# Performance work log

Hardware: AMD Instinct MI355X
Metric: run time of the kernel (lower is better)

Reference implementation:

```python
import jax, jax.numpy as jnp
import numpy as np

DIM = 1024
HID = 2048
E = 8      # num_experts
K = 2      # num_experts_per_tok


def setup_inputs() -> dict:
    key = jax.random.key(0)
    ks = jax.random.split(key, 5)
    s_in = 1.0 / np.sqrt(DIM)
    s_hid = 1.0 / np.sqrt(HID)
    x = jax.random.normal(ks[0], (2, 2048, DIM), dtype=jnp.float32)
    Wg = jax.random.uniform(ks[1], (DIM, E), minval=-s_in, maxval=s_in, dtype=jnp.float32)
    W1 = jax.random.uniform(ks[2], (E, DIM, HID), minval=-s_in, maxval=s_in, dtype=jnp.float32)
    W3 = jax.random.uniform(ks[3], (E, DIM, HID), minval=-s_in, maxval=s_in, dtype=jnp.float32)
    W2 = jax.random.uniform(ks[4], (E, HID, DIM), minval=-s_hid, maxval=s_hid, dtype=jnp.float32)
    return {"x": x, "Wg": Wg, "W1": W1, "W3": W3, "W2": W2}


def reference(x, Wg, W1, W3, W2):
    orig_shape = x.shape
    xt = x.reshape(-1, x.shape[-1])            # [T, D]
    T = xt.shape[0]
    scores = xt @ Wg                            # [T, E] (gate_softmax=False)
    ew, ei = jax.lax.top_k(scores, K)           # [T, K]
    ew = jax.nn.softmax(ew, axis=-1)            # softmax over selected experts
    # combine weights: [T, E], zero for unselected experts
    combine = jnp.zeros((T, E), dtype=xt.dtype)
    combine = combine.at[jnp.arange(T)[:, None], ei].add(ew)
    out = jnp.zeros_like(xt)
    for e in range(E):  # fixed small loop over structurally distinct experts
        h = jax.nn.silu(xt @ W1[e]) * (xt @ W3[e])   # [T, HID] SwiGLU
        out = out + combine[:, e:e + 1] * (h @ W2[e])
    return out.reshape(orig_shape)
```

## Files before the change

### kernel.cpp

```cpp
#include <hip/hip_runtime.h>

typedef unsigned short u16;
typedef unsigned int u32;
using bf16x8 = __attribute__((ext_vector_type(8))) __bf16;
using f32x4  = __attribute__((ext_vector_type(4))) float;

#define T_TOK 4096
#define DIMD  1024
#define HIDN  2048
#define NEXP  8
#define NSLOT (2 * T_TOK)

#define OFF_CNT  0
#define OFF_TCNT 64
#define OFF_TOK  16448
#define OFF_WGT  (OFF_TOK + NEXP*T_TOK*4)
#define OFF_T2S  (OFF_WGT + NEXP*T_TOK*4)
#define OFF_XB   (1<<20)
#define SZ_XB    (T_TOK*DIMD*2)
#define OFF_W1T  (OFF_XB + SZ_XB)
#define SZ_W     (NEXP*DIMD*HIDN*2)
#define OFF_W3T  (OFF_W1T + SZ_W)
#define OFF_W2T  (OFF_W3T + SZ_W)
#define OFF_H    (OFF_W2T + SZ_W)
#define OFF_OS   OFF_W1T

__device__ __forceinline__ u16 f2bf(float f) {
    u32 u = __float_as_uint(f);
    u32 r = (u + 0x7fff + ((u >> 16) & 1)) >> 16;
    return (u16)r;
}

__device__ __forceinline__ void gl2lds16(const void* g, void* l) {
    __builtin_amdgcn_global_load_lds(
        (__attribute__((address_space(1))) void*)(g),
        (__attribute__((address_space(3))) void*)(l),
        16, 0, 0);
}

__device__ __forceinline__ bf16x8 ldfrag(const u16* base, int r, int s, int q) {
    int idx = r * 64 + ((((s << 2) | q) ^ (r & 7)) << 3);
    union { uint4 u; bf16x8 b; } c;
    c.u = *(const uint4*)(base + idx);
    return c.b;
}

__device__ __forceinline__ int prefix_cnt(const int* cnt, int e) {
    int b = 0;
#pragma unroll
    for (int j = 0; j < NEXP; j++) b += (j < e) ? cnt[j] : 0;
    return b;
}

__global__ __launch_bounds__(256) void gate_kernel(
    const float* __restrict__ x, const float* __restrict__ wg,
    int* __restrict__ cnt, int* __restrict__ tok, float* __restrict__ wgt,
    u16* __restrict__ xb)
{
    int t = blockIdx.x * 4 + (threadIdx.x >> 6);
    int lane = threadIdx.x & 63;
    float s[8];
#pragma unroll
    for (int e = 0; e < 8; e++) s[e] = 0.f;
    const float* xr = x + (size_t)t * DIMD;
    u16* xbr = xb + (size_t)t * DIMD;
#pragma unroll
    for (int i = 0; i < 16; i++) {
        int d = i * 64 + lane;
        float xv = xr[d];
        xbr[d] = f2bf(xv);
        float4 w0 = *(const float4*)(wg + d * 8);
        float4 w1 = *(const float4*)(wg + d * 8 + 4);
        s[0] += xv * w0.x; s[1] += xv * w0.y;
        s[2] += xv * w0.z; s[3] += xv * w0.w;
        s[4] += xv * w1.x; s[5] += xv * w1.y;
        s[6] += xv * w1.z; s[7] += xv * w1.w;
    }
#pragma unroll
    for (int e = 0; e < 8; e++)
        for (int off = 32; off; off >>= 1) s[e] += __shfl_xor(s[e], off, 64);
    if (lane == 0) {
        int e0 = 0; float b0 = s[0];
        for (int e = 1; e < 8; e++) if (s[e] > b0) { b0 = s[e]; e0 = e; }
        int e1 = (e0 == 0) ? 1 : 0; float b1 = s[e1];
        for (int e = 0; e < 8; e++) if (e != e0 && s[e] > b1) { b1 = s[e]; e1 = e; }
        float ex = __expf(b1 - b0);
        float w0 = 1.f / (1.f + ex);
        float w1 = ex / (1.f + ex);
        int p0 = atomicAdd(&cnt[e0], 1);
        tok[e0 * T_TOK + p0] = t; wgt[e0 * T_TOK + p0] = w0;
        int p1 = atomicAdd(&cnt[e1], 1);
        tok[e1 * T_TOK + p1] = t; wgt[e1 * T_TOK + p1] = w1;
    }
}

__global__ __launch_bounds__(256) void map_kernel(
    const int* __restrict__ cnt, const int* __restrict__ tok,
    int* __restrict__ tcnt, int* __restrict__ t2s)
{
    int gid = blockIdx.x * 256 + threadIdx.x;
    int e = gid >> 12, i = gid & 4095;
    if (i >= cnt[e]) return;
    int base = prefix_cnt(cnt, e);
    int t = tok[e * T_TOK + i];
    int idx = atomicAdd(&tcnt[t], 1);
    t2s[2 * t + idx] = base + i;
}

__global__ __launch_bounds__(256) void wtr_kernel(
    const float* __restrict__ w1, u16* __restrict__ w1t,
    const float* __restrict__ w3, u16* __restrict__ w3t,
    const float* __restrict__ w2, u16* __restrict__ w2t)
{
    __shared__ float Lf[64 * 64];
    int bid = blockIdx.x;
    int tz = bid >> 9;
    int tt = bid & 511;
    int e = tz & 7;
    const float* in; u16* out; int K, N, kt, ntl;
    if (tz < 16) {
        in = (tz < 8) ? w1 : w3; out = (tz < 8) ? w1t : w3t;
        K = DIMD; N = HIDN; kt = tt >> 5; ntl = tt & 31;
    } else {
        in = w2; out = w2t;
        K = HIDN; N = DIMD; kt = tt >> 4; ntl = tt & 15;
    }
    int k0 = kt * 64, n0 = ntl * 64;
    const float* ip = in + (size_t)e * K * N;
    u16* op = out + (size_t)e * K * N;

    int tid = threadIdx.x;
    int wbase = tid & ~63;
#pragma unroll
    for (int i = 0; i < 4; i++) {
        int slot = i * 256 + tid;
        int r = slot >> 4, cb = slot & 15;
        gl2lds16(ip + (size_t)(k0 + r) * N + n0 + cb * 4,
                 Lf + (i * 256 + wbase) * 4);
    }
    __syncthreads();

    int w = tid >> 6, lane = tid & 63;
    union { u16 s[16]; uint4 q[2]; } u;
#pragma unroll
    for (int i = 0; i < 16; i++)
        u.s[i] = f2bf(Lf[(w * 16 + i) * 64 + lane]);
    uint4* dst = (uint4*)(op + (size_t)(n0 + lane) * K + k0 + w * 16);
    dst[0] = u.q[0]; dst[1] = u.q[1];
}

__global__ __launch_bounds__(256, 3) void gemm1_kernel(
    const u16* __restrict__ xb, const u16* __restrict__ w1t, const u16* __restrict__ w3t,
    const int* __restrict__ cnt, const int* __restrict__ tok,
    const float* __restrict__ wgt, u16* __restrict__ H)
{
    const int e = blockIdx.z, mt = blockIdx.y, nt = blockIdx.x;
    const int ce = cnt[e];
    if (mt * 128 >= ce) return;
    const int base = prefix_cnt(cnt, e);
    const int* tokp = tok + e * T_TOK;

    __shared__ u16 smem[128 * 64 + 64 * 64 + 64 * 64];
    u16* As  = smem;
    u16* B1s = smem + 128 * 64;
    u16* B3s = B1s + 64 * 64;

    const int tid = threadIdx.x;
    const int lane = tid & 63, q = lane >> 4, ln = lane & 15;
    const int wv = tid >> 6;
    const int wm = (wv & 1) * 64;
    const int wsel = wv >> 1;
    const int wbase = tid & ~63;

    const u16* arow[4];
#pragma unroll
    for (int i = 0; i < 4; i++) {
        int slot = i * 256 + tid;
        int m = slot >> 3;
        int bk = (slot & 7) ^ (m & 7);
        int mg = mt * 128 + m;
        int tr = (mg < ce) ? tokp[mg] : 0;
        arow[i] = xb + (size_t)tr * DIMD + bk * 8;
    }
    const u16* w1p = w1t + ((size_t)e * HIDN + nt * 64) * DIMD;
    const u16* w3p = w3t + ((size_t)e * HIDN + nt * 64) * DIMD;
    const u16* b1row[2]; const u16* b3row[2];
#pragma unroll
    for (int i = 0; i < 2; i++) {
        int slot = i * 256 + tid;
        int n = slot >> 3;
        int bk = (slot & 7) ^ (n & 7);
        b1row[i] = w1p + (size_t)n * DIMD + bk * 8;
        b3row[i] = w3p + (size_t)n * DIMD + bk * 8;
    }

    f32x4 acc[4][4];
#pragma unroll
    for (int a = 0; a < 4; a++)
#pragma unroll
        for (int b = 0; b < 4; b++) acc[a][b] = {0.f, 0.f, 0.f, 0.f};

    const u16* Bsel = wsel ? B3s : B1s;

    for (int k0 = 0; k0 < DIMD; k0 += 64) {
        __syncthreads();
#pragma unroll
        for (int i = 0; i < 4; i++)
            gl2lds16(arow[i] + k0, As + (i * 256 + wbase) * 8);
#pragma unroll
        for (int i = 0; i < 2; i++) {
            gl2lds16(b1row[i] + k0, B1s + (i * 256 + wbase) * 8);
            gl2lds16(b3row[i] + k0, B3s + (i * 256 + wbase) * 8);
        }
        __syncthreads();
#pragma unroll
        for (int s = 0; s < 2; s++) {
            bf16x8 af[4], bf[4];
#pragma unroll
            for (int mf = 0; mf < 4; mf++) af[mf] = ldfrag(As, wm + mf * 16 + ln, s, q);
#pragma unroll
            for (int nf = 0; nf < 4; nf++) bf[nf] = ldfrag(Bsel, nf * 16 + ln, s, q);
#pragma unroll
            for (int mf = 0; mf < 4; mf++)
#pragma unroll
                for (int nf = 0; nf < 4; nf++)
                    acc[mf][nf] = __builtin_amdgcn_mfma_f32_16x16x32_bf16(af[mf], bf[nf], acc[mf][nf], 0, 0, 0);
        }
    }

    __syncthreads();
    float* ex = (float*)smem;
    const int pj = wv & 1;
    if (wsel == 1) {
#pragma unroll
        for (int mf = 0; mf < 4; mf++)
#pragma unroll
            for (int nf = 0; nf < 4; nf++)
                *(f32x4*)(ex + pj * 4096 + ((mf * 4 + nf) * 64 + lane) * 4) = acc[mf][nf];
    }
    __syncthreads();
    if (wsel == 0) {
        const float* wr = wgt + e * T_TOK;
#pragma unroll
        for (int mf = 0; mf < 4; mf++) {
#pragma unroll
            for (int nf = 0; nf < 4; nf++) {
                f32x4 c2 = *(const f32x4*)(ex + pj * 4096 + ((mf * 4 + nf) * 64 + lane) * 4);
#pragma unroll
                for (int r = 0; r < 4; r++) {
                    int mg = mt * 128 + wm + mf * 16 + q * 4 + r;
                    if (mg < ce) {
                        float c1 = acc[mf][nf][r];
                        float h = (c1 / (1.f + __expf(-c1))) * c2[r] * wr[mg];
                        H[(size_t)(base + mg) * HIDN + nt * 64 + nf * 16 + ln] = f2bf(h);
                    }
                }
            }
        }
    }
}

__global__ __launch_bounds__(256, 3) void gemm2_kernel(
    const u16* __restrict__ H, const u16* __restrict__ w2t,
    const int* __restrict__ cnt, float* __restrict__ os)
{
    const int e = blockIdx.z & 7, kh = blockIdx.z >> 3;
    const int mt = blockIdx.y, nt = blockIdx.x;
    const int ce = cnt[e];
    if (mt * 128 >= ce) return;
    const int base = prefix_cnt(cnt, e);

    __shared__ u16 smem[128 * 64 * 2];
    u16* As = smem;
    u16* Bs = smem + 128 * 64;

    const int tid = threadIdx.x;
    const int lane = tid & 63, q = lane >> 4, ln = lane & 15;
    const int wv = tid >> 6;
    const int wm = (wv & 1) * 64, wn = (wv >> 1) * 64;
    const int wbase = tid & ~63;

    const u16* arow[4];
    const u16* brow[4];
    const u16* w2p = w2t + ((size_t)e * DIMD + nt * 128) * HIDN;
#pragma unroll
    for (int i = 0; i < 4; i++) {
        int slot = i * 256 + tid;
        int m = slot >> 3;
        int bk = (slot & 7) ^ (m & 7);
        int mg = mt * 128 + m;
        int ar = base + ((mg < ce) ? mg : 0);
        arow[i] = H + (size_t)ar * HIDN + bk * 8;
        brow[i] = w2p + (size_t)m * HIDN + bk * 8;
    }

    f32x4 acc[4][4];
#pragma unroll
    for (int a = 0; a < 4; a++)
#pragma unroll
        for (int b = 0; b < 4; b++) acc[a][b] = {0.f, 0.f, 0.f, 0.f};

    const int kbeg = kh * (HIDN / 2), kend = kbeg + HIDN / 2;
    for (int k0 = kbeg; k0 < kend; k0 += 64) {
        __syncthreads();
#pragma unroll
        for (int i = 0; i < 4; i++) {
            gl2lds16(arow[i] + k0, As + (i * 256 + wbase) * 8);
            gl2lds16(brow[i] + k0, Bs + (i * 256 + wbase) * 8);
        }
        __syncthreads();
#pragma unroll
        for (int s = 0; s < 2; s++) {
            bf16x8 af[4], bf[4];
#pragma unroll
            for (int mf = 0; mf < 4; mf++) af[mf] = ldfrag(As, wm + mf * 16 + ln, s, q);
#pragma unroll
            for (int nf = 0; nf < 4; nf++) bf[nf] = ldfrag(Bs, wn + nf * 16 + ln, s, q);
#pragma unroll
            for (int mf = 0; mf < 4; mf++)
#pragma unroll
                for (int nf = 0; nf < 4; nf++)
                    acc[mf][nf] = __builtin_amdgcn_mfma_f32_16x16x32_bf16(af[mf], bf[nf], acc[mf][nf], 0, 0, 0);
        }
    }

    float* osk = os + (size_t)kh * NSLOT * DIMD;
#pragma unroll
    for (int mf = 0; mf < 4; mf++) {
#pragma unroll
        for (int r = 0; r < 4; r++) {
            int mg = mt * 128 + wm + mf * 16 + q * 4 + r;
            if (mg < ce) {
                float* orow = osk + (size_t)(base + mg) * DIMD + nt * 128 + wn;
#pragma unroll
                for (int nf = 0; nf < 4; nf++)
                    orow[nf * 16 + ln] = acc[mf][nf][r];
            }
        }
    }
}

__global__ __launch_bounds__(256) void reduce_kernel(
    const float* __restrict__ os, const int* __restrict__ t2s,
    float* __restrict__ out)
{
    int t = blockIdx.x;
    int s0 = t2s[2 * t], s1 = t2s[2 * t + 1];
    int c = threadIdx.x * 4;
    const size_t khs = (size_t)NSLOT * DIMD;
    float4 a0 = *(const float4*)(os + (size_t)s0 * DIMD + c);
    float4 a1 = *(const float4*)(os + (size_t)s1 * DIMD + c);
    float4 b0 = *(const float4*)(os + khs + (size_t)s0 * DIMD + c);
    float4 b1 = *(const float4*)(os + khs + (size_t)s1 * DIMD + c);
    float4 o;
    o.x = (a0.x + a1.x) + (b0.x + b1.x);
    o.y = (a0.y + a1.y) + (b0.y + b1.y);
    o.z = (a0.z + a1.z) + (b0.z + b1.z);
    o.w = (a0.w + a1.w) + (b0.w + b1.w);
    *(float4*)(out + (size_t)t * DIMD + c) = o;
}

extern "C" void kernel_launch(void* const* d_in, const int* in_sizes, int n_in,
                              void* d_out, int out_size, void* d_ws, size_t ws_size,
                              hipStream_t stream)
{
    const float* x  = (const float*)d_in[0];
    const float* wg = (const float*)d_in[1];
    const float* w1 = (const float*)d_in[2];
    const float* w3 = (const float*)d_in[3];
    const float* w2 = (const float*)d_in[4];

    char* ws = (char*)d_ws;
    int*   cnt  = (int*)(ws + OFF_CNT);
    int*   tcnt = (int*)(ws + OFF_TCNT);
    int*   tok  = (int*)(ws + OFF_TOK);
    float* wgt  = (float*)(ws + OFF_WGT);
    int*   t2s  = (int*)(ws + OFF_T2S);
    u16*   xb   = (u16*)(ws + OFF_XB);
    u16*   w1t  = (u16*)(ws + OFF_W1T);
    u16*   w3t  = (u16*)(ws + OFF_W3T);
    u16*   w2t  = (u16*)(ws + OFF_W2T);
    u16*   Hbuf = (u16*)(ws + OFF_H);
    float* osb  = (float*)(ws + OFF_OS);
    float* outp = (float*)d_out;

    hipMemsetAsync(ws, 0, 64 + T_TOK * 4, stream);

    gate_kernel<<<T_TOK / 4, 256, 0, stream>>>(x, wg, cnt, tok, wgt, xb);
    map_kernel<<<(NEXP * T_TOK) / 256, 256, 0, stream>>>(cnt, tok, tcnt, t2s);

    wtr_kernel<<<24 * 512, 256, 0, stream>>>(w1, w1t, w3, w3t, w2, w2t);

    gemm1_kernel<<<dim3(HIDN / 64, T_TOK / 128, NEXP), 256, 0, stream>>>(
        xb, w1t, w3t, cnt, tok, wgt, Hbuf);
    gemm2_kernel<<<dim3(DIMD / 128, T_TOK / 128, NEXP * 2), 256, 0, stream>>>(
        Hbuf, w2t, cnt, osb);

    reduce_kernel<<<T_TOK, 256, 0, stream>>>(osb, t2s, outp);
}
```

Measured before the change: 506.8 us.

## Fuse gate with weight transpose and map into gemm1, enlarge transpose tiles

Merges the gating kernel and the weight conversion/transpose kernel into one launch, with the first 1024 blocks doing gating and the rest converting weights. The transpose tile grows to 128x64 so each block does twice the work. The token-to-slot map kernel moves into an extra z-slice of the gemm1 grid. Occupancy hints for both GEMMs rise from 3 to 4 waves per SIMD. Together these cut kernel launches and launch gaps, at the cost of doubling the transpose kernel's shared memory and adding register pressure in the GEMMs.

```diff
diff --git a/kernel.cpp b/kernel.cpp
--- a/kernel.cpp
+++ b/kernel.cpp
@@ -52,87 +52,79 @@
     return b;
 }
 
-__global__ __launch_bounds__(256) void gate_kernel(
+__global__ __launch_bounds__(256) void gatewtr_kernel(
     const float* __restrict__ x, const float* __restrict__ wg,
     int* __restrict__ cnt, int* __restrict__ tok, float* __restrict__ wgt,
-    u16* __restrict__ xb)
-{
-    int t = blockIdx.x * 4 + (threadIdx.x >> 6);
-    int lane = threadIdx.x & 63;
-    float s[8];
-#pragma unroll
-    for (int e = 0; e < 8; e++) s[e] = 0.f;
-    const float* xr = x + (size_t)t * DIMD;
-    u16* xbr = xb + (size_t)t * DIMD;
-#pragma unroll
-    for (int i = 0; i < 16; i++) {
-        int d = i * 64 + lane;
-        float xv = xr[d];
-        xbr[d] = f2bf(xv);
-        float4 w0 = *(const float4*)(wg + d * 8);
-        float4 w1 = *(const float4*)(wg + d * 8 + 4);
-        s[0] += xv * w0.x; s[1] += xv * w0.y;
-        s[2] += xv * w0.z; s[3] += xv * w0.w;
-        s[4] += xv * w1.x; s[5] += xv * w1.y;
-        s[6] += xv * w1.z; s[7] += xv * w1.w;
-    }
-#pragma unroll
-    for (int e = 0; e < 8; e++)
-        for (int off = 32; off; off >>= 1) s[e] += __shfl_xor(s[e], off, 64);
-    if (lane == 0) {
-        int e0 = 0; float b0 = s[0];
-        for (int e = 1; e < 8; e++) if (s[e] > b0) { b0 = s[e]; e0 = e; }
-        int e1 = (e0 == 0) ? 1 : 0; float b1 = s[e1];
-        for (int e = 0; e < 8; e++) if (e != e0 && s[e] > b1) { b1 = s[e]; e1 = e; }
-        float ex = __expf(b1 - b0);
-        float w0 = 1.f / (1.f + ex);
-        float w1 = ex / (1.f + ex);
-        int p0 = atomicAdd(&cnt[e0], 1);
-        tok[e0 * T_TOK + p0] = t; wgt[e0 * T_TOK + p0] = w0;
-        int p1 = atomicAdd(&cnt[e1], 1);
-        tok[e1 * T_TOK + p1] = t; wgt[e1 * T_TOK + p1] = w1;
-    }
-}
-
-__global__ __launch_bounds__(256) void map_kernel(
-    const int* __restrict__ cnt, const int* __restrict__ tok,
-    int* __restrict__ tcnt, int* __restrict__ t2s)
-{
-    int gid = blockIdx.x * 256 + threadIdx.x;
-    int e = gid >> 12, i = gid & 4095;
-    if (i >= cnt[e]) return;
-    int base = prefix_cnt(cnt, e);
-    int t = tok[e * T_TOK + i];
-    int idx = atomicAdd(&tcnt[t], 1);
-    t2s[2 * t + idx] = base + i;
-}
-
-__global__ __launch_bounds__(256) void wtr_kernel(
+    u16* __restrict__ xb,
     const float* __restrict__ w1, u16* __restrict__ w1t,
     const float* __restrict__ w3, u16* __restrict__ w3t,
     const float* __restrict__ w2, u16* __restrict__ w2t)
 {
-    __shared__ float Lf[64 * 64];
-    int bid = blockIdx.x;
-    int tz = bid >> 9;
-    int tt = bid & 511;
-    int e = tz & 7;
-    const float* in; u16* out; int K, N, kt, ntl;
-    if (tz < 16) {
-        in = (tz < 8) ? w1 : w3; out = (tz < 8) ? w1t : w3t;
-        K = DIMD; N = HIDN; kt = tt >> 5; ntl = tt & 31;
+    __shared__ float Lf[128 * 64];
+    const int bid = blockIdx.x;
+    const int tid = threadIdx.x;
+    const int lane = tid & 63;
+
+    if (bid < 1024) {
+        int t = bid * 4 + (tid >> 6);
+        float s[8];
+#pragma unroll
+        for (int e = 0; e < 8; e++) s[e] = 0.f;
+        const float* xr = x + (size_t)t * DIMD;
+        u16* xbr = xb + (size_t)t * DIMD;
+#pragma unroll
+        for (int i = 0; i < 16; i++) {
+            int d = i * 64 + lane;
+            float xv = xr[d];
+            xbr[d] = f2bf(xv);
+            float4 w0 = *(const float4*)(wg + d * 8);
+            float4 w1v = *(const float4*)(wg + d * 8 + 4);
+            s[0] += xv * w0.x; s[1] += xv * w0.y;
+            s[2] += xv * w0.z; s[3] += xv * w0.w;
+            s[4] += xv * w1v.x; s[5] += xv * w1v.y;
+            s[6] += xv * w1v.z; s[7] += xv * w1v.w;
+        }
+#pragma unroll
+        for (int e = 0; e < 8; e++)
+            for (int off = 32; off; off >>= 1) s[e] += __shfl_xor(s[e], off, 64);
+        if (lane == 0) {
+            int e0 = 0; float b0 = s[0];
+            for (int e = 1; e < 8; e++) if (s[e] > b0) { b0 = s[e]; e0 = e; }
+            int e1 = (e0 == 0) ? 1 : 0; float b1 = s[e1];
+            for (int e = 0; e < 8; e++) if (e != e0 && s[e] > b1) { b1 = s[e]; e1 = e; }
+            float ex = __expf(b1 - b0);
+            float w0 = 1.f / (1.f + ex);
+            float w1s = ex / (1.f + ex);
+            int p0 = atomicAdd(&cnt[e0], 1);
+            tok[e0 * T_TOK + p0] = t; wgt[e0 * T_TOK + p0] = w0;
+            int p1 = atomicAdd(&cnt[e1], 1);
+            tok[e1 * T_TOK + p1] = t; wgt[e1 * T_TOK + p1] = w1s;
+        }
+        return;
+    }
+
+    int tt = bid - 1024;
+    const float* in; u16* out; int K, N, kt, ntl, e;
+    if (tt < 4096) {
+        in = (tt < 2048) ? w1 : w3; out = (tt < 2048) ? w1t : w3t;
+        int l = tt & 2047;
+        e = l >> 8; l &= 255;
+        K = DIMD; N = HIDN;
+        kt = l >> 5; ntl = l & 31;
     } else {
         in = w2; out = w2t;
-        K = HIDN; N = DIMD; kt = tt >> 4; ntl = tt & 15;
-    }
-    int k0 = kt * 64, n0 = ntl * 64;
+        int l = tt - 4096;
+        e = l >> 8; l &= 255;
+        K = HIDN; N = DIMD;
+        kt = l >> 4; ntl = l & 15;
+    }
+    int k0 = kt * 128, n0 = ntl * 64;
     const float* ip = in + (size_t)e * K * N;
     u16* op = out + (size_t)e * K * N;
 
-    int tid = threadIdx.x;
-    int wbase = tid & ~63;
-#pragma unroll
-    for (int i = 0; i < 4; i++) {
+    const int wbase = tid & ~63;
+#pragma unroll
+    for (int i = 0; i < 8; i++) {
         int slot = i * 256 + tid;
         int r = slot >> 4, cb = slot & 15;
         gl2lds16(ip + (size_t)(k0 + r) * N + n0 + cb * 4,
@@ -140,21 +132,36 @@
     }
     __syncthreads();
 
-    int w = tid >> 6, lane = tid & 63;
-    union { u16 s[16]; uint4 q[2]; } u;
-#pragma unroll
-    for (int i = 0; i < 16; i++)
-        u.s[i] = f2bf(Lf[(w * 16 + i) * 64 + lane]);
-    uint4* dst = (uint4*)(op + (size_t)(n0 + lane) * K + k0 + w * 16);
-    dst[0] = u.q[0]; dst[1] = u.q[1];
-}
-
-__global__ __launch_bounds__(256, 3) void gemm1_kernel(
+    int w = tid >> 6;
+    union { u16 s[32]; uint4 q[4]; } u;
+#pragma unroll
+    for (int i = 0; i < 32; i++)
+        u.s[i] = f2bf(Lf[(w * 32 + i) * 64 + lane]);
+    uint4* dst = (uint4*)(op + (size_t)(n0 + lane) * K + k0 + w * 32);
+    dst[0] = u.q[0]; dst[1] = u.q[1]; dst[2] = u.q[2]; dst[3] = u.q[3];
+}
+
+__global__ __launch_bounds__(256, 4) void gemm1_kernel(
     const u16* __restrict__ xb, const u16* __restrict__ w1t, const u16* __restrict__ w3t,
     const int* __restrict__ cnt, const int* __restrict__ tok,
-    const float* __restrict__ wgt, u16* __restrict__ H)
+    const float* __restrict__ wgt, u16* __restrict__ H,
+    int* __restrict__ tcnt, int* __restrict__ t2s)
 {
     const int e = blockIdx.z, mt = blockIdx.y, nt = blockIdx.x;
+
+    if (e == NEXP) {
+        int bid1 = mt * 32 + nt;
+        if (bid1 >= 128) return;
+        int gid = bid1 * 256 + threadIdx.x;
+        int me = gid >> 12, i = gid & 4095;
+        if (i >= cnt[me]) return;
+        int base = prefix_cnt(cnt, me);
+        int t = tok[me * T_TOK + i];
+        int idx = atomicAdd(&tcnt[t], 1);
+        t2s[2 * t + idx] = base + i;
+        return;
+    }
+
     const int ce = cnt[e];
     if (mt * 128 >= ce) return;
     const int base = prefix_cnt(cnt, e);
@@ -260,7 +267,7 @@
     }
 }
 
-__global__ __launch_bounds__(256, 3) void gemm2_kernel(
+__global__ __launch_bounds__(256, 4) void gemm2_kernel(
     const u16* __restrict__ H, const u16* __restrict__ w2t,
     const int* __restrict__ cnt, float* __restrict__ os)
 {
@@ -386,13 +393,11 @@
 
     hipMemsetAsync(ws, 0, 64 + T_TOK * 4, stream);
 
-    gate_kernel<<<T_TOK / 4, 256, 0, stream>>>(x, wg, cnt, tok, wgt, xb);
-    map_kernel<<<(NEXP * T_TOK) / 256, 256, 0, stream>>>(cnt, tok, tcnt, t2s);
-
-    wtr_kernel<<<24 * 512, 256, 0, stream>>>(w1, w1t, w3, w3t, w2, w2t);
-
-    gemm1_kernel<<<dim3(HIDN / 64, T_TOK / 128, NEXP), 256, 0, stream>>>(
-        xb, w1t, w3t, cnt, tok, wgt, Hbuf);
+    gatewtr_kernel<<<1024 + 6144, 256, 0, stream>>>(
+        x, wg, cnt, tok, wgt, xb, w1, w1t, w3, w3t, w2, w2t);
+
+    gemm1_kernel<<<dim3(HIDN / 64, T_TOK / 128, NEXP + 1), 256, 0, stream>>>(
+        xb, w1t, w3t, cnt, tok, wgt, Hbuf, tcnt, t2s);
     gemm2_kernel<<<dim3(DIMD / 128, T_TOK / 128, NEXP * 2), 256, 0, stream>>>(
         Hbuf, w2t, cnt, osb);
 
```

Result: slower. 551.4 us (+8.8%).
